# Performance work log

Hardware: AMD Instinct MI355X
Metric: run time of the kernel (lower is better)

## Reference

```python
import jax, jax.numpy as jnp
import numpy as np

N_HEAD = 12
N_EMBD = 768


def setup_inputs() -> dict:
    key = jax.random.key(0)
    k1, k2, k3, k4, k5 = jax.random.split(key, 5)
    B, T, C = 4, 2048, N_EMBD
    s = 0.02
    x = jax.random.normal(k1, (B, T, C), dtype=jnp.float32)
    w_attn = jax.random.normal(k2, (C, 3 * C), dtype=jnp.float32) * s
    b_attn = jnp.zeros((3 * C,), dtype=jnp.float32)
    w_proj = jax.random.normal(k3, (C, C), dtype=jnp.float32) * s
    b_proj = jnp.zeros((C,), dtype=jnp.float32)
    return {"x": x, "w_attn": w_attn, "b_attn": b_attn, "w_proj": w_proj, "b_proj": b_proj}


def reference(x, w_attn, b_attn, w_proj, b_proj):
    # dropout omitted (eval mode / dropout=0.0)
    B, T, C = x.shape
    H = N_HEAD
    D = C // H  # head dim
    qkv = x @ w_attn + b_attn                      # [B,T,3C]
    q, k, v = jnp.split(qkv, 3, axis=-1)
    q = q.reshape(B, T, H, D).transpose(0, 2, 1, 3)  # [B,H,T,D]
    k = k.reshape(B, T, H, D).transpose(0, 2, 1, 3)
    v = v.reshape(B, T, H, D).transpose(0, 2, 1, 3)
    att = jnp.einsum('bhqd,bhkd->bhqk', q, k) * (1.0 / np.sqrt(D))  # [B,H,T,T]
    causal = jnp.tril(jnp.ones((T, T), dtype=bool))
    att = jnp.where(causal[None, None], att, -jnp.inf)
    att = jax.nn.softmax(att, axis=-1)
    y = jnp.einsum('bhqk,bhkd->bhqd', att, v)      # [B,H,T,D]
    y = y.transpose(0, 2, 1, 3).reshape(B, T, C)
    return y @ w_proj + b_proj
```

## Files before the change

### kernel.cpp

```cpp
#include <hip/hip_runtime.h>
#include <stdint.h>

typedef unsigned short ushort_t;

#define T_SEQ 2048
#define BATCH 4
#define NHEAD 12
#define CEMB 768
#define HDIM 64
#define C3 2304

__device__ __forceinline__ ushort_t f2b_hw(float f) {
  union { __bf16 h; ushort_t u; } p;
  p.h = (__bf16)f;
  return p.u;
}
__device__ __forceinline__ uint32_t pkbf16(float lo, float hi) {
  union { __bf16 h[2]; uint32_t u; } p;
  p.h[0] = (__bf16)lo; p.h[1] = (__bf16)hi;
  return p.u;
}

typedef __attribute__((address_space(3))) unsigned int lds_u32_t;
typedef const __attribute__((address_space(1))) unsigned int glb_u32_t;
__device__ __forceinline__ void async_cp16(const void* g, void* l) {
  __builtin_amdgcn_global_load_lds((glb_u32_t*)g, (lds_u32_t*)l, 16, 0, 0);
}

__global__ __launch_bounds__(256) void prep_k(const float* __restrict__ x, ushort_t* __restrict__ xb,
                                              const float* __restrict__ wa, ushort_t* __restrict__ wT,
                                              const float* __restrict__ wp, ushort_t* __restrict__ wpT) {
  const int blk = blockIdx.x;
  const int tid = threadIdx.x;
  if (blk < 3072) {
    const int i = blk * 256 + tid;
    float4 a = ((const float4*)x)[2 * i];
    float4 b = ((const float4*)x)[2 * i + 1];
    uint4 v;
    v.x = pkbf16(a.x, a.y); v.y = pkbf16(a.z, a.w);
    v.z = pkbf16(b.x, b.y); v.w = pkbf16(b.z, b.w);
    ((uint4*)xb)[i] = v;
    return;
  }
  __shared__ ushort_t tile[32][33];
  const float* in; ushort_t* out; int R, C, bx, by;
  if (blk < 4800) {
    const int t = blk - 3072;
    in = wa; out = wT; R = CEMB; C = C3;
    bx = t % 72; by = t / 72;
  } else {
    const int t = blk - 4800;
    in = wp; out = wpT; R = CEMB; C = CEMB;
    bx = t % 24; by = t / 24;
  }
  const int tx = tid & 31, ty = tid >> 5;
  const int c0 = bx * 32, r0 = by * 32;
  for (int i = ty; i < 32; i += 8)
    tile[i][tx] = f2b_hw(in[(size_t)(r0 + i) * C + c0 + tx]);
  __syncthreads();
  for (int i = ty; i < 32; i += 8)
    out[(size_t)(c0 + i) * R + r0 + tx] = tile[tx][i];
}

typedef __bf16 bf16x8 __attribute__((ext_vector_type(8)));
typedef float f32x4 __attribute__((ext_vector_type(4)));

template <bool OUTF, int BM>
__global__ __launch_bounds__(256) void gemm_bt(const ushort_t* __restrict__ A,
                                               const ushort_t* __restrict__ Bt,
                                               const float* __restrict__ bias,
                                               void* __restrict__ Cv,
                                               int M, int N, int K) {
  constexpr int TM = BM / 32;
  __shared__ ushort_t As[2][BM * 32];
  __shared__ ushort_t Bs[2][128 * 32];
  const int tid = threadIdx.x;
  const int m0 = blockIdx.y * BM, n0 = blockIdx.x * 128;
  const int wid = tid >> 6, lane = tid & 63;
  const int quad = lane >> 4, l15 = lane & 15;
  const int wm = (wid >> 1) * (BM / 2), wn = (wid & 1) * 64;
  f32x4 acc[TM][4] = {};

  const int e0 = tid * 8;
  const int r0s = e0 >> 5, c0s = e0 & 31;
  const int e1 = e0 + 2048;
  const int r1s = e1 >> 5, c1s = e1 & 31;

  const int KS = K >> 5;

#define GSTAGE(ks, bf)                                                              \
  {                                                                                 \
    const int kc = (ks) << 5;                                                       \
    async_cp16(&A[(size_t)(m0 + r0s) * K + kc + c0s], &As[bf][e0]);                 \
    if constexpr (BM == 128)                                                        \
      async_cp16(&A[(size_t)(m0 + r1s) * K + kc + c1s], &As[bf][e1]);               \
    async_cp16(&Bt[(size_t)(n0 + r0s) * K + kc + c0s], &Bs[bf][e0]);                \
    async_cp16(&Bt[(size_t)(n0 + r1s) * K + kc + c1s], &Bs[bf][e1]);                \
  }

  GSTAGE(0, 0);
  for (int ks = 0; ks < KS; ks++) {
    const int pb = ks & 1;
    __syncthreads();
    if (ks + 1 < KS) GSTAGE(ks + 1, pb ^ 1);
    bf16x8 af[TM], bfr[4];
#pragma unroll
    for (int t = 0; t < TM; t++)
      af[t] = *(const bf16x8*)&As[pb][(wm + t * 16 + l15) * 32 + quad * 8];
#pragma unroll
    for (int t = 0; t < 4; t++)
      bfr[t] = *(const bf16x8*)&Bs[pb][(wn + t * 16 + l15) * 32 + quad * 8];
#pragma unroll
    for (int tm = 0; tm < TM; tm++)
#pragma unroll
      for (int tn = 0; tn < 4; tn++)
        acc[tm][tn] = __builtin_amdgcn_mfma_f32_16x16x32_bf16(af[tm], bfr[tn], acc[tm][tn], 0, 0, 0);
  }
#undef GSTAGE

#pragma unroll
  for (int tm = 0; tm < TM; tm++) {
    const int row = m0 + wm + tm * 16 + quad * 4;
#pragma unroll
    for (int tn = 0; tn < 4; tn++) {
      const int col = n0 + wn + tn * 16 + l15;
      const float bv = bias[col];
#pragma unroll
      for (int rr = 0; rr < 4; rr++) {
        if constexpr (OUTF)
          ((float*)Cv)[(size_t)(row + rr) * N + col] = acc[tm][tn][rr] + bv;
        else
          ((ushort_t*)Cv)[(size_t)(row + rr) * N + col] = f2b_hw(acc[tm][tn][rr] + bv);
      }
    }
  }
}

#define VSTR 64

__device__ __forceinline__ void commit_v(ushort_t* __restrict__ vt, const int* __restrict__ offs,
                                         uint4 pV0, uint4 pV1) {
  union { uint32_t u[4]; uint4 v; } a, c;
  a.v = pV0; c.v = pV1;
#pragma unroll
  for (int j = 0; j < 8; j++) {
    uint32_t pk = __builtin_amdgcn_perm(c.u[j >> 1], a.u[j >> 1],
                                        (j & 1) ? 0x07060302u : 0x05040100u);
    *(uint32_t*)&vt[offs[j]] = pk;
  }
}

__global__ __launch_bounds__(256, 5) void attn_mfma_k(const ushort_t* __restrict__ qkv,
                                                      ushort_t* __restrict__ y) {
  __shared__ ushort_t Ksm[2][2][64 * 32];
  __shared__ ushort_t Vt[2][64 * VSTR];

  const int qt = 31 - blockIdx.y;
  const int h = blockIdx.x >> 2, b = blockIdx.x & 3;
  const int tid = threadIdx.x;
  const int w = tid >> 6, lane = tid & 63;
  const int quad = lane >> 4, l15 = lane & 15;
  const int nkt = qt + 1;
  const int qw = qt * 64 + w * 16;

  const int e0 = tid * 8;
  const int p_slot = tid >> 2;
  const int key_true = ((p_slot >> 5) << 5) | (((p_slot >> 2) & 3) << 3) |
                       (((p_slot >> 4) & 1) << 2) | (p_slot & 3);
  const int kchunk = (tid & 3) ^ ((p_slot >> 1) & 3);
  const ushort_t* kbase = qkv + ((size_t)(b * T_SEQ) + key_true) * C3 + CEMB + h * HDIM + kchunk * 8;
  const int vpair = tid & 31, vd0 = (tid >> 5) * 8;
  const ushort_t* vbase = qkv + ((size_t)(b * T_SEQ) + 2 * vpair) * C3 + 2 * CEMB + h * HDIM + vd0;
  const size_t step = (size_t)64 * C3;

  int voffw[8];
#pragma unroll
  for (int j = 0; j < 8; j++)
    voffw[j] = (vd0 + j) * VSTR + (((vpair >> 2) ^ j) << 3) + ((vpair & 3) << 1);

  const int sw7 = l15 & 7;
  int koff[4];
#pragma unroll
  for (int m = 0; m < 4; m++)
    koff[m] = (m * 16 + l15) * 32 + ((quad ^ ((l15 >> 1) & 3)) << 3);
  int vroff[2][4];
#pragma unroll
  for (int a2 = 0; a2 < 2; a2++)
#pragma unroll
    for (int nd = 0; nd < 4; nd++)
      vroff[a2][nd] = (nd * 16 + l15) * VSTR + (((4 * a2 + quad) ^ sw7) << 3);

  const int qrel = w * 16 + l15;

  const float C2 = 0.18033688011112042f;

  bf16x8 qB[2];
#pragma unroll
  for (int kb = 0; kb < 2; kb++)
    qB[kb] = *(const bf16x8*)&qkv[((size_t)(b * T_SEQ + qw + l15)) * C3 +
                                  h * HDIM + kb * 32 + quad * 8];

  f32x4 o2[4] = {};
  float m0 = -3e38f;
  float lq0 = 0.f;

  const ushort_t* kp = kbase;
  const ushort_t* vp = vbase;
  uint4 pV0 = *(const uint4*)vp, pV1 = *(const uint4*)(vp + C3);
  async_cp16(kp, &Ksm[0][0][e0]);
  async_cp16(kp + 32, &Ksm[0][1][e0]);
  commit_v(Vt[0], voffw, pV0, pV1);
  vp += step;
  pV0 = *(const uint4*)vp; pV1 = *(const uint4*)(vp + C3);

  for (int kt = 0; kt < nkt; ++kt) {
    __syncthreads();
    if (kt + 1 < nkt) {
      const int nb = (kt + 1) & 1;
      kp += step;
      async_cp16(kp, &Ksm[nb][0][e0]);
      async_cp16(kp + 32, &Ksm[nb][1][e0]);
      commit_v(Vt[nb], voffw, pV0, pV1);
      if (kt + 2 < nkt) {
        vp += step;
        pV0 = *(const uint4*)vp; pV1 = *(const uint4*)(vp + C3);
      }
    }
    const int cb = kt & 1;

    bf16x8 kA[4][2];
#pragma unroll
    for (int m = 0; m < 4; m++) {
      kA[m][0] = *(const bf16x8*)&Ksm[cb][0][koff[m]];
      kA[m][1] = *(const bf16x8*)&Ksm[cb][1][koff[m]];
    }
    f32x4 st0[4] = {};
#pragma unroll
    for (int m = 0; m < 4; m++) {
      st0[m] = __builtin_amdgcn_mfma_f32_16x16x32_bf16(kA[m][0], qB[0], st0[m], 0, 0, 0);
      st0[m] = __builtin_amdgcn_mfma_f32_16x16x32_bf16(kA[m][1], qB[1], st0[m], 0, 0, 0);
    }

    if (kt == nkt - 1) {
      const int kb0 = quad * 8;
#pragma unroll
      for (int m = 0; m < 4; m++) {
        const int bm = kb0 + ((m >> 1) << 5) + ((m & 1) << 2);
#pragma unroll
        for (int r = 0; r < 4; r++)
          if (bm + r > qrel) st0[m][r] = -3e38f;
      }
    }

    f32x4 mq0;
#pragma unroll
    for (int r = 0; r < 4; r++)
      mq0[r] = fmaxf(fmaxf(st0[0][r], st0[1][r]), fmaxf(st0[2][r], st0[3][r]));
    const float mx0 = fmaxf(fmaxf(mq0[0], mq0[1]), fmaxf(mq0[2], mq0[3]));

    float al0 = 1.f;
    if (__any(mx0 - m0 > 22.18f)) {
      float a = fmaxf(mx0, __shfl_xor(mx0, 16, 64));
      a = fmaxf(a, __shfl_xor(a, 32, 64));
      const float n0 = fmaxf(m0, a);
      al0 = exp2f((m0 - n0) * C2);
      m0 = n0;
#pragma unroll
      for (int nd = 0; nd < 4; nd++)
#pragma unroll
        for (int r = 0; r < 4; r++) o2[nd][r] *= al0;
    }
    const float mnc0 = m0 * C2;
#pragma unroll
    for (int m = 0; m < 4; m++)
#pragma unroll
      for (int r = 0; r < 4; r++)
        st0[m][r] = exp2f(fmaf(st0[m][r], C2, -mnc0));
    f32x4 s40;
#pragma unroll
    for (int r = 0; r < 4; r++)
      s40[r] = (st0[0][r] + st0[1][r]) + (st0[2][r] + st0[3][r]);
    lq0 = fmaf(lq0, al0, (s40[0] + s40[1]) + (s40[2] + s40[3]));

    bf16x8 pf0[2];
#pragma unroll
    for (int a2 = 0; a2 < 2; a2++) {
      union { uint32_t u[4]; bf16x8 v; } pa;
      pa.u[0] = pkbf16(st0[2 * a2][0], st0[2 * a2][1]);
      pa.u[1] = pkbf16(st0[2 * a2][2], st0[2 * a2][3]);
      pa.u[2] = pkbf16(st0[2 * a2 + 1][0], st0[2 * a2 + 1][1]);
      pa.u[3] = pkbf16(st0[2 * a2 + 1][2], st0[2 * a2 + 1][3]);
      pf0[a2] = pa.v;
    }

#pragma unroll
    for (int a2 = 0; a2 < 2; a2++)
#pragma unroll
      for (int nd = 0; nd < 4; nd++) {
        const bf16x8 vv = *(const bf16x8*)&Vt[cb][vroff[a2][nd]];
        o2[nd] = __builtin_amdgcn_mfma_f32_16x16x32_bf16(vv, pf0[a2], o2[nd], 0, 0, 0);
      }
  }

  {
    float lt0 = lq0 + __shfl_xor(lq0, 16, 64);
    lt0 += __shfl_xor(lt0, 32, 64);
    const float inv = 1.0f / lt0;
    const int qg = qw + l15;
    ushort_t* yp = y + ((size_t)(b * T_SEQ + qg)) * CEMB + h * HDIM + quad * 4;
#pragma unroll
    for (int nd = 0; nd < 4; nd++) {
      uint2 pk;
      pk.x = pkbf16(o2[nd][0] * inv, o2[nd][1] * inv);
      pk.y = pkbf16(o2[nd][2] * inv, o2[nd][3] * inv);
      *(uint2*)(yp + nd * 16) = pk;
    }
  }
}

extern "C" void kernel_launch(void* const* d_in, const int* in_sizes, int n_in,
                              void* d_out, int out_size, void* d_ws, size_t ws_size,
                              hipStream_t stream) {
  const float* x      = (const float*)d_in[0];
  const float* w_attn = (const float*)d_in[1];
  const float* b_attn = (const float*)d_in[2];
  const float* w_proj = (const float*)d_in[3];
  const float* b_proj = (const float*)d_in[4];
  float* out = (float*)d_out;

  char* ws = (char*)d_ws;
  ushort_t* qkv = (ushort_t*)ws;
  ushort_t* y   = qkv + (size_t)8192 * 2304;
  ushort_t* xb  = y + (size_t)8192 * 768;
  ushort_t* wT  = xb + (size_t)8192 * 768;
  ushort_t* wpT = wT + (size_t)2304 * 768;

  prep_k<<<5376, 256, 0, stream>>>(x, xb, w_attn, wT, w_proj, wpT);

  gemm_bt<false, 128><<<dim3(C3 / 128, 8192 / 128), 256, 0, stream>>>(xb, wT, b_attn, qkv, 8192, C3, CEMB);

  attn_mfma_k<<<dim3(48, 32), 256, 0, stream>>>(qkv, y);

  gemm_bt<true, 64><<<dim3(CEMB / 128, 8192 / 64), 256, 0, stream>>>(y, wpT, b_proj, out, 8192, CEMB, CEMB);
}
```

Before: 215.4 us.

## Triple-buffer K tiles with async copies and partial vmcnt waits

Extends the K shared-memory buffer from double to triple buffering so async K loads are issued two tiles ahead. The loop-top __syncthreads is replaced by an end-of-iteration barrier preceded by an explicit s_waitcnt with a nonzero vmcnt, so newer loads can remain in flight across iterations. Launch bounds drop from 5 to 4 blocks per CU to make room for the larger LDS footprint. This trades occupancy for deeper prefetch, and correctness now depends on the hand-counted vmcnt values matching the number of outstanding memory operations.

```diff
diff --git a/kernel.cpp b/kernel.cpp
--- a/kernel.cpp
+++ b/kernel.cpp
@@ -150,9 +150,9 @@
   }
 }
 
-__global__ __launch_bounds__(256, 5) void attn_mfma_k(const ushort_t* __restrict__ qkv,
+__global__ __launch_bounds__(256, 4) void attn_mfma_k(const ushort_t* __restrict__ qkv,
                                                       ushort_t* __restrict__ y) {
-  __shared__ ushort_t Ksm[2][2][64 * 32];
+  __shared__ ushort_t Ksm[3][2][64 * 32];
   __shared__ ushort_t Vt[2][64 * VSTR];
 
   const int qt = 31 - blockIdx.y;
@@ -209,30 +209,42 @@
   uint4 pV0 = *(const uint4*)vp, pV1 = *(const uint4*)(vp + C3);
   async_cp16(kp, &Ksm[0][0][e0]);
   async_cp16(kp + 32, &Ksm[0][1][e0]);
+  if (nkt > 1) {
+    kp += step;
+    async_cp16(kp, &Ksm[1][0][e0]);
+    async_cp16(kp + 32, &Ksm[1][1][e0]);
+  }
   commit_v(Vt[0], voffw, pV0, pV1);
-  vp += step;
-  pV0 = *(const uint4*)vp; pV1 = *(const uint4*)(vp + C3);
-
+  if (nkt > 1) {
+    vp += step;
+    pV0 = *(const uint4*)vp; pV1 = *(const uint4*)(vp + C3);
+  }
+  if (nkt > 1)
+    asm volatile("s_waitcnt vmcnt(2) lgkmcnt(0)\n\ts_barrier" ::: "memory");
+  else
+    asm volatile("s_waitcnt vmcnt(0) lgkmcnt(0)\n\ts_barrier" ::: "memory");
+
+  int cbk = 0;
   for (int kt = 0; kt < nkt; ++kt) {
-    __syncthreads();
-    if (kt + 1 < nkt) {
-      const int nb = (kt + 1) & 1;
+    if (kt + 2 < nkt) {
       kp += step;
+      const int nb = (cbk + 2 >= 3) ? cbk - 1 : cbk + 2;
       async_cp16(kp, &Ksm[nb][0][e0]);
       async_cp16(kp + 32, &Ksm[nb][1][e0]);
-      commit_v(Vt[nb], voffw, pV0, pV1);
+    }
+    if (kt + 1 < nkt) {
+      commit_v(Vt[(kt + 1) & 1], voffw, pV0, pV1);
       if (kt + 2 < nkt) {
         vp += step;
         pV0 = *(const uint4*)vp; pV1 = *(const uint4*)(vp + C3);
       }
     }
-    const int cb = kt & 1;
 
     bf16x8 kA[4][2];
 #pragma unroll
     for (int m = 0; m < 4; m++) {
-      kA[m][0] = *(const bf16x8*)&Ksm[cb][0][koff[m]];
-      kA[m][1] = *(const bf16x8*)&Ksm[cb][1][koff[m]];
+      kA[m][0] = *(const bf16x8*)&Ksm[cbk][0][koff[m]];
+      kA[m][1] = *(const bf16x8*)&Ksm[cbk][1][koff[m]];
     }
     f32x4 st0[4] = {};
 #pragma unroll
@@ -297,9 +309,15 @@
     for (int a2 = 0; a2 < 2; a2++)
 #pragma unroll
       for (int nd = 0; nd < 4; nd++) {
-        const bf16x8 vv = *(const bf16x8*)&Vt[cb][vroff[a2][nd]];
+        const bf16x8 vv = *(const bf16x8*)&Vt[kt & 1][vroff[a2][nd]];
         o2[nd] = __builtin_amdgcn_mfma_f32_16x16x32_bf16(vv, pf0[a2], o2[nd], 0, 0, 0);
       }
+
+    if (kt + 2 < nkt)
+      asm volatile("s_waitcnt vmcnt(4) lgkmcnt(0)\n\ts_barrier" ::: "memory");
+    else if (kt + 1 < nkt)
+      asm volatile("s_waitcnt vmcnt(0) lgkmcnt(0)\n\ts_barrier" ::: "memory");
+    cbk = (cbk == 2) ? 0 : cbk + 1;
   }
 
   {
```

Result: no change. 218.9 us (+1.6%).
